# Kernel tuning notes

Hardware: AMD Instinct MI355X
Metric: run time of the kernel (lower is better)

Reference implementation:

```python
import jax, jax.numpy as jnp
import numpy as np

K_NN = 32          # configs['k']
LEAKY_ALPHA = 0.2  # configs['alpha']
NHEADS = 8         # all heads share gat_W0/gat_a0 in the weights dict -> tiled output
NEG_INF = -9e15    # masked-softmax fill used by dense GAT


@jax.custom_vjp
def grad_reverse(x):
    # GradientReversalLayer: identity forward, negated gradient backward
    return x

def _gr_fwd(x):
    return x, None

def _gr_bwd(res, g):
    return (-g,)

grad_reverse.defvjp(_gr_fwd, _gr_bwd)


def setup_inputs() -> dict:
    key = jax.random.key(0)
    ks = jax.random.split(key, 11)
    N, D = 6144, 512           # N = (num_domains+1)*batch_size = 4*1536
    H1, H2, G = 256, 128, 64   # hidden_layers=[256,128], gat_hidden=[64]
    C, ND = 16, 3              # num_classes, num source-domain discriminators

    def xav(k, shape):
        limit = np.float32(np.sqrt(6.0 / (shape[0] + shape[1])) * 1.414)
        return jax.random.uniform(k, shape, jnp.float32, -limit, limit)

    return {
        "x": jax.random.normal(ks[0], (N, D), jnp.float32),
        "fc_W0": xav(ks[1], (D, H1)),
        "fc_b0": jax.random.normal(ks[2], (H1,), jnp.float32) * 0.01,
        "fc_W1": xav(ks[3], (H1, H2)),
        "fc_b1": jax.random.normal(ks[4], (H2,), jnp.float32) * 0.01,
        "gat_W": xav(ks[5], (H2, G)),
        "gat_a": jax.random.normal(ks[6], (2 * G, 1), jnp.float32) * 0.1,
        "cls_W": xav(ks[7], (NHEADS * G, C)),
        "cls_b": jax.random.normal(ks[8], (C,), jnp.float32) * 0.01,
        "dsc_W": jax.random.uniform(ks[9], (ND, NHEADS * G, 2), jnp.float32),
        "dsc_b": jax.random.uniform(ks[10], (ND, 2), jnp.float32),
    }


def reference(x, fc_W0, fc_b0, fc_W1, fc_b1, gat_W, gat_a, cls_W, cls_b, dsc_W, dsc_b):
    # --- feature extractor MLP (Linear 'fc' + relu), dropout=0 / eval mode ---
    h = jax.nn.relu(x @ fc_W0 + fc_b0)
    h = jax.nn.relu(h @ fc_W1 + fc_b1)          # [N, 128]
    n = h.shape[0]

    # --- AdjacencyLayer / DistanceLayer: kNN over pairwise L2 distances ---
    sq = jnp.sum(h * h, axis=1)
    d2 = sq[:, None] + sq[None, :] - 2.0 * (h @ h.T)      # [N, N] squared dists
    d2 = d2 + jnp.eye(n, dtype=h.dtype) * 1e9             # exclude self from kNN
    _, idx = jax.lax.top_k(-jax.lax.stop_gradient(d2), K_NN)  # [N, K]
    adj = jnp.zeros((n, n), h.dtype).at[jnp.arange(n)[:, None], idx].set(1.0)
    adj = adj + jnp.eye(n, dtype=h.dtype)                 # self loops

    # --- dense GraphAttentionLayer (single shared head, tiled nheads times) ---
    Wh = h @ gat_W                                        # [N, G]
    Gd = Wh.shape[1]
    f1 = Wh @ gat_a[:Gd]                                  # [N, 1]
    f2 = Wh @ gat_a[Gd:]                                  # [N, 1]
    e = jax.nn.leaky_relu(f1 + f2.T, LEAKY_ALPHA)         # [N, N]
    att = jax.nn.softmax(jnp.where(adj > 0, e, NEG_INF), axis=1)
    hp = jax.nn.elu(att @ Wh)                             # [N, G]
    gat_out = jnp.tile(hp, (1, NHEADS))                   # concat of shared heads

    # --- class head + domain discriminators behind gradient reversal ---
    cls_logits = gat_out @ cls_W + cls_b                  # [N, C]
    rev = grad_reverse(gat_out)
    dsc_logits = jnp.einsum('nd,kdo->nko', rev, dsc_W) + dsc_b  # [N, ND, 2]
    return jnp.concatenate([cls_logits, dsc_logits.reshape(n, -1)], axis=1)
```

## Files before the change

### kernel.cpp

```cpp
#include <hip/hip_runtime.h>
#include <float.h>

#define N_PTS 6144
#define D_IN  512
#define H1_DIM 256
#define H2_DIM 128
#define G_DIM  64
#define KNN    32
#define NOUT   22

typedef short s8v __attribute__((ext_vector_type(8)));
typedef float f32x4 __attribute__((ext_vector_type(4)));
typedef unsigned u32x4 __attribute__((ext_vector_type(4)));
typedef unsigned short u16;
typedef unsigned short u16x4 __attribute__((ext_vector_type(4)));
typedef unsigned long long u64;

__device__ __forceinline__ u16 f2bf(float f) {
  unsigned u = __float_as_uint(f);
  u += 0x7FFFu + ((u >> 16) & 1u);
  return (u16)(u >> 16);
}
__device__ __forceinline__ float bf2f(u16 s) {
  return __uint_as_float(((unsigned)s) << 16);
}
__device__ __forceinline__ void split3(float v, u16& a0, u16& a1, u16& a2) {
  a0 = f2bf(v);
  float r1 = v - bf2f(a0);
  a1 = f2bf(r1);
  a2 = f2bf(r1 - bf2f(a1));
}
__device__ __forceinline__ unsigned sortkey(float f) {
  unsigned ub = __float_as_uint(f);
  return (ub & 0x80000000u) ? ~ub : (ub | 0x80000000u);
}

template<int BM, bool AF32, bool SPLITK, bool BIAS, bool RELU, bool WF32, bool WSPLIT, bool WKEY, bool SYMM>
__global__ __launch_bounds__(256, 4) void mfma_gemm(
    const void* __restrict__ A0any, const u16* __restrict__ A1_, const u16* __restrict__ A2_,
    const u16* __restrict__ B0_, const u16* __restrict__ B1_, const u16* __restrict__ B2_,
    const float* __restrict__ bias,
    float* __restrict__ Cf, u16* __restrict__ C0, u16* __restrict__ C1, u16* __restrict__ C2,
    int Ktot, int Ks, int ldC, size_t MN, int rowoff)
{
  if (SYMM) {
    if ((int)(blockIdx.x >> 1) < (int)blockIdx.y) return;
  }
  const int MT = BM / 32, NT = 2;
  const int APL = BM * 32;
  const int BBASE = 3 * APL;
  __shared__ u16 lds[(BM + 64) * 32 * 3];

  const int t = threadIdx.x;
  const int lane = t & 63, wave = t >> 6;
  const int wm = wave >> 1, wn = wave & 1;
  const int m0 = blockIdx.y * BM, n0 = blockIdx.x * 64;
  const int kz = blockIdx.z * Ks;

  f32x4 acc[MT][NT] = {};

  const int pA = BM / 16;
  const int NC = 3 * pA + 12;

  for (int k0 = 0; k0 < Ks; k0 += 32) {
    if (k0) __syncthreads();
    const int kb = kz + k0;
    if (AF32) {
      const float* A = (const float*)A0any;
      #pragma unroll
      for (int c0 = 0; c0 < BM * 4; c0 += 256) {
        int c = c0 + t;
        int row = c >> 2, slot = c & 3;
        const float* g = A + (size_t)(m0 + row) * Ktot + kb + slot * 8;
        f32x4 fa = *(const f32x4*)g;
        f32x4 fb = *(const f32x4*)(g + 4);
        int dst = row * 32 + ((slot ^ ((row >> 1) & 3)) << 3);
        s8v v0, v1, v2;
        #pragma unroll
        for (int e = 0; e < 4; ++e) {
          u16 a0, a1, a2; split3(fa[e], a0, a1, a2);
          v0[e] = (short)a0; v1[e] = (short)a1; v2[e] = (short)a2;
        }
        #pragma unroll
        for (int e = 0; e < 4; ++e) {
          u16 a0, a1, a2; split3(fb[e], a0, a1, a2);
          v0[4 + e] = (short)a0; v1[4 + e] = (short)a1; v2[4 + e] = (short)a2;
        }
        *(s8v*)(lds + dst) = v0;
        *(s8v*)(lds + APL + dst) = v1;
        *(s8v*)(lds + 2 * APL + dst) = v2;
      }
      for (int c = wave; c < 12; c += 4) {
        int p = c >> 2, lc = c & 3;
        int row = lc * 16 + (lane >> 2);
        int srcslot = (lane & 3) ^ ((row >> 1) & 3);
        const u16* src = (p == 0) ? B0_ : (p == 1) ? B1_ : B2_;
        const u16* g = src + (size_t)(n0 + row) * Ktot + kb + srcslot * 8;
        __builtin_amdgcn_global_load_lds(
            (const __attribute__((address_space(1))) unsigned*)g,
            (__attribute__((address_space(3))) unsigned*)(lds + BBASE + p * 2048 + lc * 512),
            16, 0, 0);
      }
    } else {
      for (int c = wave; c < NC; c += 4) {
        const u16* src; int dstoff; int row0; int lc;
        if (c < 3 * pA) {
          int p = c / pA; lc = c % pA;
          src = (p == 0) ? (const u16*)A0any : (p == 1) ? A1_ : A2_;
          dstoff = p * APL + lc * 512;
          row0 = m0;
        } else {
          int cb = c - 3 * pA;
          int p = cb >> 2; lc = cb & 3;
          src = (p == 0) ? B0_ : (p == 1) ? B1_ : B2_;
          dstoff = BBASE + p * 2048 + lc * 512;
          row0 = n0;
        }
        int row = lc * 16 + (lane >> 2);
        int srcslot = (lane & 3) ^ ((row >> 1) & 3);
        const u16* g = src + (size_t)(row0 + row) * Ktot + kb + srcslot * 8;
        __builtin_amdgcn_global_load_lds(
            (const __attribute__((address_space(1))) unsigned*)g,
            (__attribute__((address_space(3))) unsigned*)(lds + dstoff),
            16, 0, 0);
      }
    }
    __syncthreads();

    s8v af[3][MT], bf[3][NT];
    #pragma unroll
    for (int mt = 0; mt < MT; ++mt) {
      int r = wm * (BM / 2) + mt * 16 + (lane & 15);
      int off = r * 32 + (((lane >> 4) ^ ((r >> 1) & 3)) << 3);
      #pragma unroll
      for (int p = 0; p < 3; ++p) af[p][mt] = *(const s8v*)(lds + p * APL + off);
    }
    #pragma unroll
    for (int nt = 0; nt < NT; ++nt) {
      int r = wn * 32 + nt * 16 + (lane & 15);
      int off = r * 32 + (((lane >> 4) ^ ((r >> 1) & 3)) << 3);
      #pragma unroll
      for (int p = 0; p < 3; ++p) bf[p][nt] = *(const s8v*)(lds + BBASE + p * 2048 + off);
    }
    #pragma unroll
    for (int mt = 0; mt < MT; ++mt)
      #pragma unroll
      for (int nt = 0; nt < NT; ++nt) {
        f32x4 a = acc[mt][nt];
        a = __builtin_amdgcn_mfma_f32_16x16x32_bf16(af[0][mt], bf[0][nt], a, 0, 0, 0);
        a = __builtin_amdgcn_mfma_f32_16x16x32_bf16(af[0][mt], bf[1][nt], a, 0, 0, 0);
        a = __builtin_amdgcn_mfma_f32_16x16x32_bf16(af[1][mt], bf[0][nt], a, 0, 0, 0);
        a = __builtin_amdgcn_mfma_f32_16x16x32_bf16(af[1][mt], bf[1][nt], a, 0, 0, 0);
        a = __builtin_amdgcn_mfma_f32_16x16x32_bf16(af[0][mt], bf[2][nt], a, 0, 0, 0);
        a = __builtin_amdgcn_mfma_f32_16x16x32_bf16(af[2][mt], bf[0][nt], a, 0, 0, 0);
        acc[mt][nt] = a;
      }
  }

  if (WKEY) {
    const bool mirror = SYMM && ((int)(blockIdx.x >> 1) > (int)blockIdx.y);
    u16 mk[MT][NT][4];
    __syncthreads();
    u16* stD = lds;
    #pragma unroll
    for (int mt = 0; mt < MT; ++mt) {
      #pragma unroll
      for (int nt = 0; nt < NT; ++nt) {
        int cl = wn * 32 + nt * 16 + (lane & 15);
        float sqc = bias[n0 + cl];
        #pragma unroll
        for (int v = 0; v < 4; ++v) {
          int rl = wm * (BM / 2) + mt * 16 + (lane >> 4) * 4 + v;
          float val = acc[mt][nt][v];
          float f = fmaf(-2.f, val, sqc);
          unsigned uu = sortkey(f);
          if (rowoff + m0 + rl == n0 + cl) uu = 0xFFFFFFFFu;
          stD[rl * 72 + cl] = (u16)(uu >> 16);
          if (mirror) {
            float fm = fmaf(-2.f, val, bias[m0 + rl]);
            mk[mt][nt][v] = (u16)(sortkey(fm) >> 16);
          }
        }
      }
    }
    __syncthreads();
    u16* Cu = (u16*)Cf;
    for (int e = t; e < BM * 8; e += 256) {
      int row = e >> 3, ch = e & 7;
      u32x4 vv = *(const u32x4*)(stD + row * 72 + ch * 8);
      *(u32x4*)(Cu + (size_t)(m0 + row) * ldC + n0 + ch * 8) = vv;
    }
    if (mirror) {
      __syncthreads();
      u16* stM = lds;
      #pragma unroll
      for (int mt = 0; mt < MT; ++mt) {
        #pragma unroll
        for (int nt = 0; nt < NT; ++nt) {
          int cl = wn * 32 + nt * 16 + (lane & 15);
          #pragma unroll
          for (int v = 0; v < 4; ++v) {
            int rl = wm * (BM / 2) + mt * 16 + (lane >> 4) * 4 + v;
            stM[cl * 136 + rl] = mk[mt][nt][v];
          }
        }
      }
      __syncthreads();
      for (int e = t; e < 64 * 16; e += 256) {
        int row = e >> 4, ch = e & 15;
        u32x4 vv = *(const u32x4*)(stM + row * 136 + ch * 8);
        *(u32x4*)(Cu + (size_t)(n0 + row) * ldC + m0 + ch * 8) = vv;
      }
    }
    return;
  }

  #pragma unroll
  for (int mt = 0; mt < MT; ++mt) {
    #pragma unroll
    for (int nt = 0; nt < NT; ++nt) {
      int col = n0 + wn * 32 + nt * 16 + (lane & 15);
      float bv = (BIAS && !SPLITK) ? bias[col] : 0.f;
      #pragma unroll
      for (int v = 0; v < 4; ++v) {
        int row = m0 + wm * (BM / 2) + mt * 16 + (lane >> 4) * 4 + v;
        float val = acc[mt][nt][v] + bv;
        size_t o = (size_t)row * ldC + col;
        if (SPLITK) {
          Cf[(size_t)blockIdx.z * MN + o] = val;
        } else {
          if (RELU) val = fmaxf(val, 0.f);
          if (WF32) Cf[o] = val;
          if (WSPLIT) {
            u16 a0, a1, a2; split3(val, a0, a1, a2);
            C0[o] = a0; C1[o] = a1; C2[o] = a2;
          }
        }
      }
    }
  }
}

template<int S, bool BIAS, bool RELU, bool WF32, bool WSPLIT>
__global__ void combine(const float* __restrict__ P, const float* __restrict__ bias,
                        size_t MN, int Ncols,
                        float* __restrict__ Cf, u16* __restrict__ C0,
                        u16* __restrict__ C1, u16* __restrict__ C2)
{
  size_t idx = ((size_t)blockIdx.x * 256 + threadIdx.x) * 4;
  if (idx >= MN) return;
  f32x4 s = *(const f32x4*)(P + idx);
  #pragma unroll
  for (int z = 1; z < S; ++z) s += *(const f32x4*)(P + (size_t)z * MN + idx);
  int n = (int)(idx % (size_t)Ncols);
  #pragma unroll
  for (int e = 0; e < 4; ++e) {
    float v = s[e] + (BIAS ? bias[n + e] : 0.f);
    if (RELU) v = fmaxf(v, 0.f);
    if (WF32) Cf[idx + e] = v;
    if (WSPLIT) {
      u16 a0, a1, a2; split3(v, a0, a1, a2);
      C0[idx + e] = a0; C1[idx + e] = a1; C2[idx + e] = a2;
    }
  }
}

__global__ void prep_all(const float* __restrict__ W0, u16* __restrict__ a0,
                         u16* __restrict__ a1, u16* __restrict__ a2,
                         const float* __restrict__ W1, u16* __restrict__ b0,
                         u16* __restrict__ b1, u16* __restrict__ b2,
                         const float* __restrict__ gW, u16* __restrict__ c0,
                         u16* __restrict__ c1, u16* __restrict__ c2,
                         const float* __restrict__ cW, const float* __restrict__ cb,
                         const float* __restrict__ dW, const float* __restrict__ db,
                         float* __restrict__ Wc, float* __restrict__ bc)
{
  int id = blockIdx.x * 256 + threadIdx.x;
  const int S0 = D_IN * H1_DIM, S1 = H1_DIM * H2_DIM, S2 = H2_DIM * G_DIM;
  const int SW = S0 + S1 + S2;
  if (id < SW) {
    const float* W; u16 *p0, *p1, *p2; int K, N;
    if (id < S0)           { W = W0; p0 = a0; p1 = a1; p2 = a2; K = D_IN;   N = H1_DIM; }
    else if (id < S0 + S1) { id -= S0; W = W1; p0 = b0; p1 = b1; p2 = b2; K = H1_DIM; N = H2_DIM; }
    else                   { id -= S0 + S1; W = gW; p0 = c0; p1 = c1; p2 = c2; K = H2_DIM; N = G_DIM; }
    int k = id / N, n = id % N;
    u16 x0, x1, x2;
    split3(W[id], x0, x1, x2);
    size_t o = (size_t)n * K + k;
    p0[o] = x0; p1[o] = x1; p2[o] = x2;
    return;
  }
  id -= SW;
  if (id < 64 * NOUT) {
    int g = id / NOUT, c = id % NOUT;
    float s = 0.f;
    if (c < 16) {
      for (int r = 0; r < 8; ++r) s += cW[(r * 64 + g) * 16 + c];
    } else {
      int k = (c - 16) >> 1, o = (c - 16) & 1;
      for (int r = 0; r < 8; ++r) s += dW[k * 1024 + (r * 64 + g) * 2 + o];
    }
    Wc[id] = s;
    if (g == 0) bc[c] = (c < 16) ? cb[c] : db[c - 16];
  }
}

__global__ void row_stats(const float* __restrict__ h, const float* __restrict__ Wh,
                          const float* __restrict__ ga, float* __restrict__ sq,
                          float* __restrict__ f1, float* __restrict__ f2)
{
  int i = blockIdx.x * 256 + threadIdx.x;
  const float* hr = h + (size_t)i * H2_DIM;
  float s = 0.f;
  for (int k = 0; k < H2_DIM; ++k) { float v = hr[k]; s = fmaf(v, v, s); }
  sq[i] = s;
  const float* wr = Wh + (size_t)i * G_DIM;
  float a = 0.f, b = 0.f;
  for (int g = 0; g < G_DIM; ++g) {
    float w = wr[g];
    a = fmaf(w, ga[g], a);
    b = fmaf(w, ga[G_DIM + g], b);
  }
  f1[i] = a; f2[i] = b;
}

__global__ __launch_bounds__(256) void topk_att(const u16* __restrict__ Sb,
    const float* __restrict__ f1, const float* __restrict__ f2,
    const float* __restrict__ Wh, const float* __restrict__ Wc, const float* __restrict__ bc,
    const float* __restrict__ sq, const float* __restrict__ hF,
    float* __restrict__ out, int m0, int nrows)
{
  const int t = threadIdx.x;
  const int lane = t & 63, wv = t >> 6;
  const int row4 = (nrows - 4 - blockIdx.x * 4) + wv;
  const int i = m0 + row4;
  const u16* Srow = Sb + (size_t)row4 * N_PTS;

  __shared__ float WcL[64 * NOUT];
  __shared__ unsigned candS[4][384];
  __shared__ u16 tieS[4][128];
  __shared__ float hiL[4][128];
  __shared__ int neighS[4][33];
  __shared__ float attS[4][33];
  __shared__ float hpfS[4][64];

  for (int idx = t; idx < 64 * NOUT; idx += 256) WcL[idx] = Wc[idx];
  __syncthreads();

  hiL[wv][lane]      = hF[(size_t)i * H2_DIM + lane];
  hiL[wv][64 + lane] = hF[(size_t)i * H2_DIM + 64 + lane];

  unsigned q[24];
  #pragma unroll
  for (int c = 0; c < 24; ++c) {
    u16x4 v = *(const u16x4*)(Srow + (c << 8) + (lane << 2));
    unsigned a = v[0] < v[1] ? (unsigned)v[0] : (unsigned)v[1];
    unsigned b = v[2] < v[3] ? (unsigned)v[2] : (unsigned)v[3];
    q[c] = a < b ? a : b;
  }

  unsigned lmin = q[0];
  #pragma unroll
  for (int c = 1; c < 24; ++c) lmin = q[c] < lmin ? q[c] : lmin;

  unsigned mnl = lmin, mxl = lmin;
  #pragma unroll
  for (int off = 32; off > 0; off >>= 1) {
    unsigned o1 = __shfl_xor(mnl, off); mnl = o1 < mnl ? o1 : mnl;
    unsigned o2 = __shfl_xor(mxl, off); mxl = o2 > mxl ? o2 : mxl;
  }

  long long lo = (long long)mnl - 1, hi = (long long)mxl;
  while (hi - lo > 1) {
    long long span = hi - lo;
    unsigned m1 = (unsigned)(lo + (span >> 2));
    unsigned m2 = (unsigned)(lo + (span >> 1));
    unsigned m3 = (unsigned)(hi - (span >> 2));
    int c1 = 0, c2 = 0, c3 = 0;
    #pragma unroll
    for (int c = 0; c < 24; ++c) {
      c1 += (q[c] <= m1);
      c2 += (q[c] <= m2);
      c3 += (q[c] <= m3);
    }
    #pragma unroll
    for (int off = 32; off > 0; off >>= 1) {
      c1 += __shfl_xor(c1, off);
      c2 += __shfl_xor(c2, off);
      c3 += __shfl_xor(c3, off);
    }
    if (c1 >= KNN)       { hi = m1; }
    else if (c2 >= KNN)  { lo = m1; hi = m2; }
    else if (c3 >= KNN)  { lo = m2; hi = m3; }
    else                 { lo = m3; }
  }
  const unsigned Q = (unsigned)hi;

  #pragma unroll
  for (int s = 0; s < 6; ++s) candS[wv][lane + s * 64] = 0xFFFFFFFFu;
  const u64 below = (lane == 0) ? 0ull : (~0ull >> (64 - lane));
  int qcnt = 0;
  #pragma unroll
  for (int c = 0; c < 24; ++c) {
    bool act = (q[c] <= Q);
    u64 mask = __ballot(act);
    if (act) {
      int pos = qcnt + (int)__popcll(mask & below);
      if (pos < 96) {
        u16x4 v = *(const u16x4*)(Srow + (c << 8) + (lane << 2));
        #pragma unroll
        for (int e = 0; e < 4; ++e) {
          int j = (c << 8) + (lane << 2) + e;
          candS[wv][pos * 4 + e] = ((unsigned)v[e] << 13) | (unsigned)j;
        }
      }
    }
    qcnt += (int)__popcll(mask);
  }

  unsigned ck[6];
  #pragma unroll
  for (int s = 0; s < 6; ++s) ck[s] = candS[wv][lane + s * 64];

  lo = -1; hi = 0x10000;
  while (hi - lo > 1) {
    long long span = hi - lo;
    unsigned m1 = (unsigned)(lo + (span >> 2));
    unsigned m2 = (unsigned)(lo + (span >> 1));
    unsigned m3 = (unsigned)(hi - (span >> 2));
    int c1 = 0, c2 = 0, c3 = 0;
    #pragma unroll
    for (int s = 0; s < 6; ++s) {
      unsigned k = ck[s] >> 13;
      c1 += (k <= m1);
      c2 += (k <= m2);
      c3 += (k <= m3);
    }
    #pragma unroll
    for (int off = 32; off > 0; off >>= 1) {
      c1 += __shfl_xor(c1, off);
      c2 += __shfl_xor(c2, off);
      c3 += __shfl_xor(c3, off);
    }
    if (c1 >= KNN)       { hi = m1; }
    else if (c2 >= KNN)  { lo = m1; hi = m2; }
    else if (c3 >= KNN)  { lo = m2; hi = m3; }
    else                 { lo = m3; }
  }
  const unsigned T = (unsigned)hi;

  int sA = 0, sB = 0;
  #pragma unroll
  for (int s = 0; s < 6; ++s) {
    unsigned k = ck[s] >> 13;
    bool strict = (k < T);
    u64 ms = __ballot(strict);
    if (strict) {
      int pos = sA + (int)__popcll(ms & below);
      if (pos < 32) neighS[wv][pos] = (int)(ck[s] & 0x1FFFu);
    }
    sA += (int)__popcll(ms);
    bool tie = (k == T);
    u64 mt2 = __ballot(tie);
    if (tie) {
      int pos = sB + (int)__popcll(mt2 & below);
      if (pos < 128) tieS[wv][pos] = (u16)(ck[s] & 0x1FFFu);
    }
    sB += (int)__popcll(mt2);
  }
  if (sB > 128) sB = 128;
  const int need = KNN - sA;

  u64 r0 = ~0ull, r1 = ~0ull;
  const float* hi0 = &hiL[wv][0];
  #pragma unroll
  for (int half = 0; half < 2; ++half) {
    int e = lane + half * 64;
    if (e < sB) {
      int j = tieS[wv][e];
      const float* hj = hF + (size_t)j * H2_DIM;
      float dot = 0.f;
      for (int d = 0; d < H2_DIM; d += 4) {
        f32x4 a = *(const f32x4*)(hi0 + d);
        f32x4 b = *(const f32x4*)(hj + d);
        dot = fmaf(a[0], b[0], fmaf(a[1], b[1], fmaf(a[2], b[2], fmaf(a[3], b[3], dot))));
      }
      float f = fmaf(-2.f, dot, sq[j]);
      u64 rk = ((u64)sortkey(f) << 13) | (unsigned)j;
      if (half == 0) r0 = rk; else r1 = rk;
    }
  }

  {
    candS[wv][lane] = (unsigned)(r0 >> 32); candS[wv][64 + lane] = (unsigned)r0;
    candS[wv][128 + lane] = (unsigned)(r1 >> 32); candS[wv][192 + lane] = (unsigned)r1;
    u64 v0 = ((u64)candS[wv][(2 * lane) >= 64 ? 128 + (2 * lane - 64) : 2 * lane] << 32)
           | candS[wv][(2 * lane) >= 64 ? 192 + (2 * lane - 64) : 64 + 2 * lane];
    u64 v1 = ((u64)candS[wv][(2 * lane + 1) >= 64 ? 128 + (2 * lane + 1 - 64) : 2 * lane + 1] << 32)
           | candS[wv][(2 * lane + 1) >= 64 ? 192 + (2 * lane + 1 - 64) : 64 + 2 * lane + 1];
    const int e0 = 2 * lane, e1 = e0 + 1;
    for (int k = 2; k <= 128; k <<= 1) {
      for (int j = k >> 1; j >= 2; j >>= 1) {
        int half = j >> 1;
        u64 o0 = __shfl_xor(v0, half);
        u64 o1 = __shfl_xor(v1, half);
        bool up0 = ((e0 & k) == 0) == ((e0 & j) == 0);
        bool up1 = ((e1 & k) == 0) == ((e1 & j) == 0);
        v0 = up0 ? (v0 < o0 ? v0 : o0) : (v0 > o0 ? v0 : o0);
        v1 = up1 ? (v1 < o1 ? v1 : o1) : (v1 > o1 ? v1 : o1);
      }
      bool asc = ((e0 & k) == 0);
      u64 a = v0 < v1 ? v0 : v1, b = v0 < v1 ? v1 : v0;
      v0 = asc ? a : b;
      v1 = asc ? b : a;
    }
    if (e0 < need) neighS[wv][sA + e0] = (int)(v0 & 0x1FFFu);
    if (e1 < need) neighS[wv][sA + e1] = (int)(v1 & 0x1FFFu);
  }
  if (lane == 0) neighS[wv][32] = i;

  {
    float e = -FLT_MAX;
    if (lane < 33) {
      float raw = f1[i] + f2[neighS[wv][lane]];
      e = raw > 0.f ? raw : 0.2f * raw;
    }
    float mx = e;
    #pragma unroll
    for (int off = 32; off > 0; off >>= 1) mx = fmaxf(mx, __shfl_xor(mx, off));
    float ex = (lane < 33) ? expf(e - mx) : 0.f;
    float sm = ex;
    #pragma unroll
    for (int off = 32; off > 0; off >>= 1) sm += __shfl_xor(sm, off);
    if (lane < 33) attS[wv][lane] = ex / sm;
  }

  {
    float s = 0.f;
    for (int m = 0; m < 33; ++m)
      s = fmaf(attS[wv][m], Wh[(size_t)neighS[wv][m] * G_DIM + lane], s);
    hpfS[wv][lane] = s > 0.f ? s : expm1f(s);
  }

  if (lane < NOUT) {
    float o = bc[lane];
    for (int g = 0; g < 64; ++g) o = fmaf(hpfS[wv][g], WcL[g * NOUT + lane], o);
    out[(size_t)i * NOUT + lane] = o;
  }
}

extern "C" void kernel_launch(void* const* d_in, const int* in_sizes, int n_in,
                              void* d_out, int out_size, void* d_ws, size_t ws_size,
                              hipStream_t stream)
{
  const float* x  = (const float*)d_in[0];
  const float* W0 = (const float*)d_in[1];
  const float* b0 = (const float*)d_in[2];
  const float* W1 = (const float*)d_in[3];
  const float* b1 = (const float*)d_in[4];
  const float* gW = (const float*)d_in[5];
  const float* ga = (const float*)d_in[6];
  const float* cW = (const float*)d_in[7];
  const float* cb = (const float*)d_in[8];
  const float* dW = (const float*)d_in[9];
  const float* db = (const float*)d_in[10];
  float* out = (float*)d_out;

  char* base = (char*)d_ws;
  char* w = base;
  auto alloc = [&](size_t bytes) { char* p = w; w += (bytes + 255) & ~(size_t)255; return p; };
  u16 *W0p[3], *W1p[3], *gWp[3], *h1p[3], *hp[3];
  for (int p = 0; p < 3; ++p) W0p[p] = (u16*)alloc((size_t)D_IN * H1_DIM * 2);
  for (int p = 0; p < 3; ++p) W1p[p] = (u16*)alloc((size_t)H1_DIM * H2_DIM * 2);
  for (int p = 0; p < 3; ++p) gWp[p] = (u16*)alloc((size_t)H2_DIM * G_DIM * 2);
  for (int p = 0; p < 3; ++p) h1p[p] = (u16*)alloc((size_t)N_PTS * H1_DIM * 2);
  for (int p = 0; p < 3; ++p) hp[p]  = (u16*)alloc((size_t)N_PTS * H2_DIM * 2);
  float* hF  = (float*)alloc((size_t)N_PTS * H2_DIM * 4);
  float* WhF = (float*)alloc((size_t)N_PTS * G_DIM * 4);
  float* sqv = (float*)alloc(N_PTS * 4);
  float* f1v = (float*)alloc(N_PTS * 4);
  float* f2v = (float*)alloc(N_PTS * 4);
  float* Wc  = (float*)alloc(64 * NOUT * 4);
  float* bc  = (float*)alloc(64 * 4);

  char* pbase = w;
  const size_t MN1 = (size_t)N_PTS * H1_DIM;
  const size_t MN2 = (size_t)N_PTS * H2_DIM;
  const size_t MN3 = (size_t)N_PTS * G_DIM;
  float* P1 = (float*)alloc(4 * MN1 * 4);
  float* P2 = (float*)alloc(4 * MN2 * 4);
  float* P3 = (float*)alloc(4 * MN3 * 4);
  u16* Sb = (u16*)pbase;

  size_t used_persist = (size_t)(pbase - base);
  size_t avail16 = (ws_size > used_persist) ? (ws_size - used_persist) / 2 : 0;
  int rowblk = 128;
  const int rcand[] = {6144, 3072, 1536, 768, 384, 256, 128};
  for (int c : rcand) { if ((size_t)c * N_PTS <= avail16) { rowblk = c; break; } }

  const int TS = D_IN * H1_DIM + H1_DIM * H2_DIM + H2_DIM * G_DIM + 64 * NOUT;
  prep_all<<<(TS + 255) / 256, 256, 0, stream>>>(
      W0, W0p[0], W0p[1], W0p[2], W1, W1p[0], W1p[1], W1p[2], gW, gWp[0], gWp[1], gWp[2],
      cW, cb, dW, db, Wc, bc);

  mfma_gemm<64, true, true, false, false, false, false, false, false>
      <<<dim3(H1_DIM / 64, N_PTS / 64, 4), 256, 0, stream>>>(
      x, nullptr, nullptr, W0p[0], W0p[1], W0p[2], nullptr,
      P1, nullptr, nullptr, nullptr, D_IN, D_IN / 4, H1_DIM, MN1, 0);
  combine<4, true, true, false, true><<<(int)(MN1 / 1024), 256, 0, stream>>>(
      P1, b0, MN1, H1_DIM, nullptr, h1p[0], h1p[1], h1p[2]);

  mfma_gemm<64, false, true, false, false, false, false, false, false>
      <<<dim3(H2_DIM / 64, N_PTS / 64, 4), 256, 0, stream>>>(
      h1p[0], h1p[1], h1p[2], W1p[0], W1p[1], W1p[2], nullptr,
      P2, nullptr, nullptr, nullptr, H1_DIM, H1_DIM / 4, H2_DIM, MN2, 0);
  combine<4, true, true, true, true><<<(int)(MN2 / 1024), 256, 0, stream>>>(
      P2, b1, MN2, H2_DIM, hF, hp[0], hp[1], hp[2]);

  mfma_gemm<64, false, true, false, false, false, false, false, false>
      <<<dim3(G_DIM / 64, N_PTS / 64, 4), 256, 0, stream>>>(
      hp[0], hp[1], hp[2], gWp[0], gWp[1], gWp[2], nullptr,
      P3, nullptr, nullptr, nullptr, H2_DIM, H2_DIM / 4, G_DIM, MN3, 0);
  combine<4, false, false, true, false><<<(int)(MN3 / 1024), 256, 0, stream>>>(
      P3, nullptr, MN3, G_DIM, WhF, nullptr, nullptr, nullptr);

  row_stats<<<N_PTS / 256, 256, 0, stream>>>(hF, WhF, ga, sqv, f1v, f2v);

  if (rowblk == N_PTS) {
    mfma_gemm<128, false, false, false, false, false, false, true, true>
        <<<dim3(N_PTS / 64, N_PTS / 128, 1), 256, 0, stream>>>(
        hp[0], hp[1], hp[2], hp[0], hp[1], hp[2], sqv,
        (float*)Sb, nullptr, nullptr, nullptr, H2_DIM, H2_DIM, N_PTS, 0, 0);
    topk_att<<<N_PTS / 4, 256, 0, stream>>>(Sb, f1v, f2v, WhF, Wc, bc, sqv, hF, out, 0, N_PTS);
  } else {
    for (int b = 0; b < N_PTS / rowblk; ++b) {
      mfma_gemm<128, false, false, false, false, false, false, true, false>
          <<<dim3(N_PTS / 64, rowblk / 128, 1), 256, 0, stream>>>(
          hp[0] + (size_t)b * rowblk * H2_DIM, hp[1] + (size_t)b * rowblk * H2_DIM,
          hp[2] + (size_t)b * rowblk * H2_DIM, hp[0], hp[1], hp[2], sqv,
          (float*)Sb, nullptr, nullptr, nullptr, H2_DIM, H2_DIM, N_PTS, 0, b * rowblk);
      topk_att<<<rowblk / 4, 256, 0, stream>>>(Sb, f1v, f2v, WhF, Wc, bc, sqv, hF, out, b * rowblk, rowblk);
    }
  }
}
```

Baseline: 170.7 us.

## Add dedicated symmetric 128x128 Gram kernel for kNN distance keys

```diff
diff --git a/kernel.cpp b/kernel.cpp
--- a/kernel.cpp
+++ b/kernel.cpp
@@ -35,17 +35,14 @@
   return (ub & 0x80000000u) ? ~ub : (ub | 0x80000000u);
 }
 
-template<int BM, bool AF32, bool SPLITK, bool BIAS, bool RELU, bool WF32, bool WSPLIT, bool WKEY, bool SYMM>
+template<int BM, bool AF32, bool SPLITK, bool BIAS, bool RELU, bool WF32, bool WSPLIT>
 __global__ __launch_bounds__(256, 4) void mfma_gemm(
     const void* __restrict__ A0any, const u16* __restrict__ A1_, const u16* __restrict__ A2_,
     const u16* __restrict__ B0_, const u16* __restrict__ B1_, const u16* __restrict__ B2_,
     const float* __restrict__ bias,
     float* __restrict__ Cf, u16* __restrict__ C0, u16* __restrict__ C1, u16* __restrict__ C2,
-    int Ktot, int Ks, int ldC, size_t MN, int rowoff)
+    int Ktot, int Ks, int ldC, size_t MN)
 {
-  if (SYMM) {
-    if ((int)(blockIdx.x >> 1) < (int)blockIdx.y) return;
-  }
   const int MT = BM / 32, NT = 2;
   const int APL = BM * 32;
   const int BBASE = 3 * APL;
@@ -157,64 +154,6 @@
       }
   }
 
-  if (WKEY) {
-    const bool mirror = SYMM && ((int)(blockIdx.x >> 1) > (int)blockIdx.y);
-    u16 mk[MT][NT][4];
-    __syncthreads();
-    u16* stD = lds;
-    #pragma unroll
-    for (int mt = 0; mt < MT; ++mt) {
-      #pragma unroll
-      for (int nt = 0; nt < NT; ++nt) {
-        int cl = wn * 32 + nt * 16 + (lane & 15);
-        float sqc = bias[n0 + cl];
-        #pragma unroll
-        for (int v = 0; v < 4; ++v) {
-          int rl = wm * (BM / 2) + mt * 16 + (lane >> 4) * 4 + v;
-          float val = acc[mt][nt][v];
-          float f = fmaf(-2.f, val, sqc);
-          unsigned uu = sortkey(f);
-          if (rowoff + m0 + rl == n0 + cl) uu = 0xFFFFFFFFu;
-          stD[rl * 72 + cl] = (u16)(uu >> 16);
-          if (mirror) {
-            float fm = fmaf(-2.f, val, bias[m0 + rl]);
-            mk[mt][nt][v] = (u16)(sortkey(fm) >> 16);
-          }
-        }
-      }
-    }
-    __syncthreads();
-    u16* Cu = (u16*)Cf;
-    for (int e = t; e < BM * 8; e += 256) {
-      int row = e >> 3, ch = e & 7;
-      u32x4 vv = *(const u32x4*)(stD + row * 72 + ch * 8);
-      *(u32x4*)(Cu + (size_t)(m0 + row) * ldC + n0 + ch * 8) = vv;
-    }
-    if (mirror) {
-      __syncthreads();
-      u16* stM = lds;
-      #pragma unroll
-      for (int mt = 0; mt < MT; ++mt) {
-        #pragma unroll
-        for (int nt = 0; nt < NT; ++nt) {
-          int cl = wn * 32 + nt * 16 + (lane & 15);
-          #pragma unroll
-          for (int v = 0; v < 4; ++v) {
-            int rl = wm * (BM / 2) + mt * 16 + (lane >> 4) * 4 + v;
-            stM[cl * 136 + rl] = mk[mt][nt][v];
-          }
-        }
-      }
-      __syncthreads();
-      for (int e = t; e < 64 * 16; e += 256) {
-        int row = e >> 4, ch = e & 15;
-        u32x4 vv = *(const u32x4*)(stM + row * 136 + ch * 8);
-        *(u32x4*)(Cu + (size_t)(n0 + row) * ldC + m0 + ch * 8) = vv;
-      }
-    }
-    return;
-  }
-
   #pragma unroll
   for (int mt = 0; mt < MT; ++mt) {
     #pragma unroll
@@ -237,6 +176,128 @@
           }
         }
       }
+    }
+  }
+}
+
+__global__ __launch_bounds__(256, 3) void gram_symm(
+    const u16* __restrict__ A0, const u16* __restrict__ A1, const u16* __restrict__ A2,
+    const float* __restrict__ sq, u16* __restrict__ Ck, int ldC)
+{
+  if ((int)blockIdx.x < (int)blockIdx.y) return;
+  const int MT = 4, NT = 4;
+  __shared__ u16 lds[2 * 128 * 32 * 3];
+
+  const int t = threadIdx.x;
+  const int lane = t & 63, wave = t >> 6;
+  const int wm = wave >> 1, wn = wave & 1;
+  const int m0 = blockIdx.y * 128, n0 = blockIdx.x * 128;
+  const bool mirror = (int)blockIdx.x > (int)blockIdx.y;
+
+  f32x4 acc[MT][NT] = {};
+
+  for (int k0 = 0; k0 < H2_DIM; k0 += 32) {
+    if (k0) __syncthreads();
+    for (int c = wave; c < 48; c += 4) {
+      int half = c >= 24;
+      int cb = half ? c - 24 : c;
+      int p = cb >> 3, lc = cb & 7;
+      const u16* src = (p == 0) ? A0 : (p == 1) ? A1 : A2;
+      int dstoff = half * 12288 + p * 4096 + lc * 512;
+      int row0 = half ? n0 : m0;
+      int row = lc * 16 + (lane >> 2);
+      int srcslot = (lane & 3) ^ ((row >> 1) & 3);
+      const u16* g = src + (size_t)(row0 + row) * H2_DIM + k0 + srcslot * 8;
+      __builtin_amdgcn_global_load_lds(
+          (const __attribute__((address_space(1))) unsigned*)g,
+          (__attribute__((address_space(3))) unsigned*)(lds + dstoff),
+          16, 0, 0);
+    }
+    __syncthreads();
+
+    s8v af[3][MT], bf[3][NT];
+    #pragma unroll
+    for (int mt = 0; mt < MT; ++mt) {
+      int r = wm * 64 + mt * 16 + (lane & 15);
+      int off = r * 32 + (((lane >> 4) ^ ((r >> 1) & 3)) << 3);
+      #pragma unroll
+      for (int p = 0; p < 3; ++p) af[p][mt] = *(const s8v*)(lds + p * 4096 + off);
+    }
+    #pragma unroll
+    for (int nt = 0; nt < NT; ++nt) {
+      int r = wn * 64 + nt * 16 + (lane & 15);
+      int off = r * 32 + (((lane >> 4) ^ ((r >> 1) & 3)) << 3);
+      #pragma unroll
+      for (int p = 0; p < 3; ++p) bf[p][nt] = *(const s8v*)(lds + 12288 + p * 4096 + off);
+    }
+    #pragma unroll
+    for (int mt = 0; mt < MT; ++mt)
+      #pragma unroll
+      for (int nt = 0; nt < NT; ++nt) {
+        f32x4 a = acc[mt][nt];
+        a = __builtin_amdgcn_mfma_f32_16x16x32_bf16(af[0][mt], bf[0][nt], a, 0, 0, 0);
+        a = __builtin_amdgcn_mfma_f32_16x16x32_bf16(af[0][mt], bf[1][nt], a, 0, 0, 0);
+        a = __builtin_amdgcn_mfma_f32_16x16x32_bf16(af[1][mt], bf[0][nt], a, 0, 0, 0);
+        a = __builtin_amdgcn_mfma_f32_16x16x32_bf16(af[1][mt], bf[1][nt], a, 0, 0, 0);
+        a = __builtin_amdgcn_mfma_f32_16x16x32_bf16(af[0][mt], bf[2][nt], a, 0, 0, 0);
+        a = __builtin_amdgcn_mfma_f32_16x16x32_bf16(af[2][mt], bf[0][nt], a, 0, 0, 0);
+        acc[mt][nt] = a;
+      }
+  }
+
+  unsigned mk32[MT][NT][2];
+  __syncthreads();
+  u16* stD = lds;
+  #pragma unroll
+  for (int mt = 0; mt < MT; ++mt) {
+    #pragma unroll
+    for (int nt = 0; nt < NT; ++nt) {
+      int cl = wn * 64 + nt * 16 + (lane & 15);
+      float sqc = sq[n0 + cl];
+      #pragma unroll
+      for (int v = 0; v < 4; ++v) {
+        int rl = wm * 64 + mt * 16 + (lane >> 4) * 4 + v;
+        float val = acc[mt][nt][v];
+        float f = fmaf(-2.f, val, sqc);
+        unsigned uu = sortkey(f);
+        if (m0 + rl == n0 + cl) uu = 0xFFFFFFFFu;
+        stD[rl * 136 + cl] = (u16)(uu >> 16);
+        if (mirror) {
+          unsigned km = sortkey(fmaf(-2.f, val, sq[m0 + rl])) >> 16;
+          if (v & 1) mk32[mt][nt][v >> 1] |= km << 16;
+          else       mk32[mt][nt][v >> 1] = km;
+        }
+      }
+    }
+  }
+  __syncthreads();
+  for (int e = t; e < 128 * 16; e += 256) {
+    int row = e >> 4, ch = e & 15;
+    u32x4 vv = *(const u32x4*)(stD + row * 136 + ch * 8);
+    *(u32x4*)(Ck + (size_t)(m0 + row) * ldC + n0 + ch * 8) = vv;
+  }
+  if (mirror) {
+    __syncthreads();
+    u16* stM = lds;
+    #pragma unroll
+    for (int mt = 0; mt < MT; ++mt) {
+      #pragma unroll
+      for (int nt = 0; nt < NT; ++nt) {
+        int cl = wn * 64 + nt * 16 + (lane & 15);
+        #pragma unroll
+        for (int v = 0; v < 4; ++v) {
+          int rl = wm * 64 + mt * 16 + (lane >> 4) * 4 + v;
+          unsigned km = (v & 1) ? (mk32[mt][nt][v >> 1] >> 16)
+                                : (mk32[mt][nt][v >> 1] & 0xFFFFu);
+          stM[cl * 136 + rl] = (u16)km;
+        }
+      }
+    }
+    __syncthreads();
+    for (int e = t; e < 128 * 16; e += 256) {
+      int row = e >> 4, ch = e & 15;
+      u32x4 vv = *(const u32x4*)(stM + row * 136 + ch * 8);
+      *(u32x4*)(Ck + (size_t)(n0 + row) * ldC + m0 + ch * 8) = vv;
     }
   }
 }
@@ -594,52 +655,43 @@
 
   size_t used_persist = (size_t)(pbase - base);
   size_t avail16 = (ws_size > used_persist) ? (ws_size - used_persist) / 2 : 0;
-  int rowblk = 128;
-  const int rcand[] = {6144, 3072, 1536, 768, 384, 256, 128};
-  for (int c : rcand) { if ((size_t)c * N_PTS <= avail16) { rowblk = c; break; } }
+  bool fullSb = ((size_t)N_PTS * N_PTS <= avail16);
 
   const int TS = D_IN * H1_DIM + H1_DIM * H2_DIM + H2_DIM * G_DIM + 64 * NOUT;
   prep_all<<<(TS + 255) / 256, 256, 0, stream>>>(
       W0, W0p[0], W0p[1], W0p[2], W1, W1p[0], W1p[1], W1p[2], gW, gWp[0], gWp[1], gWp[2],
       cW, cb, dW, db, Wc, bc);
 
-  mfma_gemm<64, true, true, false, false, false, false, false, false>
+  mfma_gemm<64, true, true, false, false, false, false>
       <<<dim3(H1_DIM / 64, N_PTS / 64, 4), 256, 0, stream>>>(
       x, nullptr, nullptr, W0p[0], W0p[1], W0p[2], nullptr,
-      P1, nullptr, nullptr, nullptr, D_IN, D_IN / 4, H1_DIM, MN1, 0);
+      P1, nullptr, nullptr, nullptr, D_IN, D_IN / 4, H1_DIM, MN1);
   combine<4, true, true, false, true><<<(int)(MN1 / 1024), 256, 0, stream>>>(
       P1, b0, MN1, H1_DIM, nullptr, h1p[0], h1p[1], h1p[2]);
 
-  mfma_gemm<64, false, true, false, false, false, false, false, false>
+  mfma_gemm<64, false, true, false, false, false, false>
       <<<dim3(H2_DIM / 64, N_PTS / 64, 4), 256, 0, stream>>>(
       h1p[0], h1p[1], h1p[2], W1p[0], W1p[1], W1p[2], nullptr,
-      P2, nullptr, nullptr, nullptr, H1_DIM, H1_DIM / 4, H2_DIM, MN2, 0);
+      P2, nullptr, nullptr, nullptr, H1_DIM, H1_DIM / 4, H2_DIM, MN2);
   combine<4, true, true, true, true><<<(int)(MN2 / 1024), 256, 0, stream>>>(
       P2, b1, MN2, H2_DIM, hF, hp[0], hp[1], hp[2]);
 
-  mfma_gemm<64, false, true, false, false, false, false, false, false>
+  mfma_gemm<64, false, true, false, false, false, false>
       <<<dim3(G_DIM / 64, N_PTS / 64, 4), 256, 0, stream>>>(
       hp[0], hp[1], hp[2], gWp[0], gWp[1], gWp[2], nullptr,
-      P3, nullptr, nullptr, nullptr, H2_DIM, H2_DIM / 4, G_DIM, MN3, 0);
+      P3, nullptr, nullptr, nullptr, H2_DIM, H2_DIM / 4, G_DIM, MN3);
   combine<4, false, false, true, false><<<(int)(MN3 / 1024), 256, 0, stream>>>(
       P3, nullptr, MN3, G_DIM, WhF, nullptr, nullptr, nullptr);
 
   row_stats<<<N_PTS / 256, 256, 0, stream>>>(hF, WhF, ga, sqv, f1v, f2v);
 
-  if (rowblk == N_PTS) {
-    mfma_gemm<128, false, false, false, false, false, false, true, true>
-        <<<dim3(N_PTS / 64, N_PTS / 128, 1), 256, 0, stream>>>(
-        hp[0], hp[1], hp[2], hp[0], hp[1], hp[2], sqv,
-        (float*)Sb, nullptr, nullptr, nullptr, H2_DIM, H2_DIM, N_PTS, 0, 0);
+  if (fullSb) {
+    gram_symm<<<dim3(N_PTS / 128, N_PTS / 128), 256, 0, stream>>>(
+        hp[0], hp[1], hp[2], sqv, Sb, N_PTS);
     topk_att<<<N_PTS / 4, 256, 0, stream>>>(Sb, f1v, f2v, WhF, Wc, bc, sqv, hF, out, 0, N_PTS);
   } else {
-    for (int b = 0; b < N_PTS / rowblk; ++b) {
-      mfma_gemm<128, false, false, false, false, false, false, true, false>
-          <<<dim3(N_PTS / 64, rowblk / 128, 1), 256, 0, stream>>>(
-          hp[0] + (size_t)b * rowblk * H2_DIM, hp[1] + (size_t)b * rowblk * H2_DIM,
-          hp[2] + (size_t)b * rowblk * H2_DIM, hp[0], hp[1], hp[2], sqv,
-          (float*)Sb, nullptr, nullptr, nullptr, H2_DIM, H2_DIM, N_PTS, 0, b * rowblk);
-      topk_att<<<rowblk / 4, 256, 0, stream>>>(Sb, f1v, f2v, WhF, Wc, bc, sqv, hF, out, b * rowblk, rowblk);
-    }
-  }
-}
+    gram_symm<<<dim3(N_PTS / 128, N_PTS / 128), 256, 0, stream>>>(
+        hp[0], hp[1], hp[2], sqv, Sb, N_PTS);
+    topk_att<<<N_PTS / 4, 256, 0, stream>>>(Sb, f1v, f2v, WhF, Wc, bc, sqv, hF, out, 0, N_PTS);
+  }
+}
```

New measurement: 168.9 us. No clear change (-1.0%).
